# Kernel optimization log

Hardware: AMD Instinct MI355X
Metric: run time of the kernel (lower is better)

Reference implementation:

```python
import jax, jax.numpy as jnp
import numpy as np

D_MODEL = 1024
N_HEADS = 16
HEAD_DIM = D_MODEL // N_HEADS  # 64
TOP_K = 64
EPS = 1e-12  # matches F.normalize eps


def setup_inputs() -> dict:
    key = jax.random.key(0)
    ks = jax.random.split(key, 6)
    s = 0.02
    def w(k):
        return jax.random.normal(k, (D_MODEL, D_MODEL), jnp.float32) * s
    zb = jnp.zeros((D_MODEL,), jnp.float32)
    # x: (B, T, d_model); T must equal d_model (see compress_proj constraint)
    x = jax.random.normal(ks[0], (2, 1024, D_MODEL), jnp.float32)
    return {
        "x": x,
        "Wq": w(ks[1]), "bq": zb,
        "Wk": w(ks[2]), "bk": zb,
        "Wv": w(ks[3]), "bv": zb,
        "Wo": w(ks[4]), "bo": zb,
        "Wc": w(ks[5]), "bc": zb,  # compress_proj (applied along time axis)
    }


def _l2norm(a):
    n = jnp.linalg.norm(a, axis=-1, keepdims=True)
    return a / jnp.maximum(n, EPS)


def reference(x, Wq, bq, Wk, bk, Wv, bv, Wo, bo, Wc, bc):
    B, T, Dm = x.shape
    H, hd = N_HEADS, HEAD_DIM

    def proj(W, b):
        return (x @ W.T + b).reshape(B, T, H, hd).transpose(0, 2, 1, 3)  # (B,H,T,hd)

    Q = proj(Wq, bq)
    K = proj(Wk, bk)
    V = proj(Wv, bv)

    # compress_kv with compress_ratio=1: compress_proj acts on the (transposed)
    # time axis, so K_comp[b,h,c,d] = sum_t K[b,h,t,d] * Wc[c,t] + bc[c]
    K_comp = jnp.einsum('bhtd,ct->bhcd', K, Wc) + bc[None, None, :, None]
    V_comp = jnp.einsum('bhtd,ct->bhcd', V, Wc) + bc[None, None, :, None]

    # lightning indexer: cosine similarity + top-k over compressed slots
    sim = jnp.einsum('bhtd,bhcd->bhtc', _l2norm(Q), _l2norm(K_comp))
    topk_idx = jax.lax.top_k(sim, TOP_K)[1]  # (B,H,T,K)

    bi = jnp.arange(B)[:, None, None, None]
    hi = jnp.arange(H)[None, :, None, None]
    K_sel = K_comp[bi, hi, topk_idx]  # (B,H,T,K,hd)
    V_sel = V_comp[bi, hi, topk_idx]

    scores = jnp.einsum('bhtd,bhtkd->bhtk', Q, K_sel) / float(np.sqrt(hd))
    attn = jax.nn.softmax(scores, axis=-1)
    out = jnp.einsum('bhtk,bhtkd->bhtd', attn, V_sel)  # (B,H,T,hd)
    out = out.transpose(0, 2, 1, 3).reshape(B, T, Dm)
    return out @ Wo.T + bo
```

## Files before the change

kernel.cpp:

```cpp
#include <hip/hip_runtime.h>
#include <type_traits>


#define DEVI __device__ __forceinline__

constexpr int Tn = 1024;
constexpr int Cn = 1024;
constexpr int Hn = 16;

typedef short bf16x8 __attribute__((ext_vector_type(8)));
typedef float f32x4 __attribute__((ext_vector_type(4)));

DEVI int wsumi(int v)   { for (int m = 1; m < 64; m <<= 1) v += __shfl_xor(v, m); return v; }
DEVI int wmini(int v)   { for (int m = 1; m < 64; m <<= 1) { int o = __shfl_xor(v, m); v = o < v ? o : v; } return v; }
DEVI float wfmax(float v){ for (int m = 1; m < 64; m <<= 1) v = fmaxf(v, __shfl_xor(v, m)); return v; }
DEVI float wfsum(float v){ for (int m = 1; m < 64; m <<= 1) v += __shfl_xor(v, m); return v; }

DEVI unsigned long long mapd(double x) {
  unsigned long long b = (unsigned long long)__double_as_longlong(x);
  return (b >> 63) ? ~b : (b | 0x8000000000000000ull);
}

DEVI unsigned short f2bf_rne(float x) {
  unsigned u = __float_as_uint(x);
  u += 0x7fffu + ((u >> 16) & 1u);
  return (unsigned short)(u >> 16);
}
struct BfPair { short hi, lo; };
DEVI BfPair split2(float x) {
  unsigned short h = f2bf_rne(x);
  float hf = __uint_as_float(((unsigned)h) << 16);
  BfPair r;
  r.hi = (short)h;
  r.lo = (short)f2bf_rne(x - hf);
  return r;
}

template <typename OUTT, typename ACCT, bool BTRANS, int BIASMODE, bool SIM>
__global__ __launch_bounds__(256) void gemm_k(
    const float* __restrict__ A, const float* __restrict__ B,
    const float* __restrict__ bias, OUTT* __restrict__ C,
    int Kd, int lda, int ldb, int ldc,
    long long zA, long long zB, long long zC, int group_base)
{
  __shared__ float As[16][68];
  __shared__ float Bs[16][68];

  size_t offA, offB, offC;
  if (SIM) {
    int pair = group_base + (int)blockIdx.z;
    int bb = pair >> 4, hh = pair & 15;
    offA = ((size_t)bb * Tn) * (size_t)lda + (size_t)hh * 64;
    offB = ((size_t)bb * Cn) * (size_t)ldb + (size_t)hh * 64;
    offC = (size_t)blockIdx.z * (size_t)Tn * (size_t)ldc;
  } else {
    offA = (size_t)blockIdx.z * (size_t)zA;
    offB = (size_t)blockIdx.z * (size_t)zB;
    offC = (size_t)blockIdx.z * (size_t)zC;
  }
  const float* Ab = A + offA;
  const float* Bb = B + offB;
  OUTT* Cb = C + offC;

  const int tid = threadIdx.x;
  const int tx = tid & 15, ty = tid >> 4;
  const int m0 = blockIdx.y * 64, n0 = blockIdx.x * 64;

  ACCT acc[4][4];
#pragma unroll
  for (int i = 0; i < 4; ++i)
#pragma unroll
    for (int j = 0; j < 4; ++j) acc[i][j] = (ACCT)0;

  for (int k0 = 0; k0 < Kd; k0 += 16) {
    {
      int m = tid >> 2, kf = tid & 3;
      float4 a = *(const float4*)(Ab + (size_t)(m0 + m) * lda + k0 + 4 * kf);
      As[4 * kf + 0][m] = a.x; As[4 * kf + 1][m] = a.y;
      As[4 * kf + 2][m] = a.z; As[4 * kf + 3][m] = a.w;
    }
    if (BTRANS) {
      int n = tid >> 2, kf = tid & 3;
      float4 b = *(const float4*)(Bb + (size_t)(n0 + n) * ldb + k0 + 4 * kf);
      Bs[4 * kf + 0][n] = b.x; Bs[4 * kf + 1][n] = b.y;
      Bs[4 * kf + 2][n] = b.z; Bs[4 * kf + 3][n] = b.w;
    } else {
      int k = tid >> 4, nf = tid & 15;
      float4 b = *(const float4*)(Bb + (size_t)(k0 + k) * ldb + n0 + 4 * nf);
      *(float4*)&Bs[k][4 * nf] = b;
    }
    __syncthreads();
#pragma unroll
    for (int k = 0; k < 16; ++k) {
      float4 a4 = *(const float4*)&As[k][4 * ty];
      float4 b4 = *(const float4*)&Bs[k][4 * tx];
      float av[4] = {a4.x, a4.y, a4.z, a4.w};
      float bv[4] = {b4.x, b4.y, b4.z, b4.w};
#pragma unroll
      for (int i = 0; i < 4; ++i)
#pragma unroll
        for (int j = 0; j < 4; ++j)
          acc[i][j] += (ACCT)av[i] * (ACCT)bv[j];
    }
    __syncthreads();
  }

  if constexpr (std::is_same<OUTT, double>::value) {
#pragma unroll
    for (int i = 0; i < 4; ++i) {
      size_t m = (size_t)(m0 + 4 * ty + i);
      double* p = (double*)Cb + m * ldc + n0 + 4 * tx;
      p[0] = (double)acc[i][0]; p[1] = (double)acc[i][1];
      p[2] = (double)acc[i][2]; p[3] = (double)acc[i][3];
    }
  } else {
    float cbv[4] = {0.f, 0.f, 0.f, 0.f};
    if (BIASMODE == 1) {
      float4 b4 = *(const float4*)(bias + n0 + 4 * tx);
      cbv[0] = b4.x; cbv[1] = b4.y; cbv[2] = b4.z; cbv[3] = b4.w;
    }
#pragma unroll
    for (int i = 0; i < 4; ++i) {
      int m = m0 + 4 * ty + i;
      float rb = (BIASMODE == 2) ? bias[m] : 0.f;
      float4 s;
      s.x = (float)acc[i][0] + cbv[0] + rb;
      s.y = (float)acc[i][1] + cbv[1] + rb;
      s.z = (float)acc[i][2] + cbv[2] + rb;
      s.w = (float)acc[i][3] + cbv[3] + rb;
      *(float4*)((float*)Cb + (size_t)m * ldc + n0 + 4 * tx) = s;
    }
  }
}

__global__ __launch_bounds__(256) void presplit2_k(
    const float* __restrict__ src, short* __restrict__ hi,
    short* __restrict__ lo, int n8)
{
  int stride = (int)gridDim.x * 256;
  for (int i = (int)blockIdx.x * 256 + (int)threadIdx.x; i < n8; i += stride) {
    float4 v0 = ((const float4*)src)[2 * i];
    float4 v1 = ((const float4*)src)[2 * i + 1];
    BfPair q0 = split2(v0.x), q1 = split2(v0.y), q2 = split2(v0.z), q3 = split2(v0.w);
    BfPair q4 = split2(v1.x), q5 = split2(v1.y), q6 = split2(v1.z), q7 = split2(v1.w);
    bf16x8 h = {q0.hi, q1.hi, q2.hi, q3.hi, q4.hi, q5.hi, q6.hi, q7.hi};
    bf16x8 l = {q0.lo, q1.lo, q2.lo, q3.lo, q4.lo, q5.lo, q6.lo, q7.lo};
    ((bf16x8*)hi)[i] = h;
    ((bf16x8*)lo)[i] = l;
  }
}

__global__ __launch_bounds__(256) void bfgemm_k(
    const short* __restrict__ Ahi, const short* __restrict__ Alo,
    const short* __restrict__ Bhi, const short* __restrict__ Blo,
    const float* __restrict__ bias, float* __restrict__ C,
    int Kd, int lda, int ldb, int ldc)
{
  __shared__ short Ah[4 * 64 * 8];
  __shared__ short Al[4 * 64 * 8];
  __shared__ short Bh[4 * 64 * 8];
  __shared__ short Bl[4 * 64 * 8];

  const int tid = threadIdx.x;
  const int lane = tid & 63, w = tid >> 6;
  const int wr = w >> 1, wc = w & 1;
  const int m0 = blockIdx.y * 64, n0 = blockIdx.x * 64;
  const int r16 = lane & 15, kg = lane >> 4;

  f32x4 acc[2][2];
#pragma unroll
  for (int i = 0; i < 2; ++i)
#pragma unroll
    for (int j = 0; j < 2; ++j) acc[i][j] = (f32x4){0.f, 0.f, 0.f, 0.f};

  const int row = tid >> 2, kseg = tid & 3;
  const int sidx = (kseg * 64 + row) * 8;

  for (int k0 = 0; k0 < Kd; k0 += 32) {
    size_t ao = (size_t)(m0 + row) * lda + k0 + kseg * 8;
    size_t bo = (size_t)(n0 + row) * ldb + k0 + kseg * 8;
    *(bf16x8*)&Ah[sidx] = *(const bf16x8*)(Ahi + ao);
    *(bf16x8*)&Al[sidx] = *(const bf16x8*)(Alo + ao);
    *(bf16x8*)&Bh[sidx] = *(const bf16x8*)(Bhi + bo);
    *(bf16x8*)&Bl[sidx] = *(const bf16x8*)(Blo + bo);
    __syncthreads();

    bf16x8 ah[2], al[2], bh[2], bl[2];
#pragma unroll
    for (int f = 0; f < 2; ++f) {
      int ia = (kg * 64 + wr * 32 + f * 16 + r16) * 8;
      int ib = (kg * 64 + wc * 32 + f * 16 + r16) * 8;
      ah[f] = *(const bf16x8*)&Ah[ia];
      al[f] = *(const bf16x8*)&Al[ia];
      bh[f] = *(const bf16x8*)&Bh[ib];
      bl[f] = *(const bf16x8*)&Bl[ib];
    }
#pragma unroll
    for (int fr = 0; fr < 2; ++fr)
#pragma unroll
      for (int fc = 0; fc < 2; ++fc) {
        f32x4 c = acc[fr][fc];
        c = __builtin_amdgcn_mfma_f32_16x16x32_bf16(al[fr], bh[fc], c, 0, 0, 0);
        c = __builtin_amdgcn_mfma_f32_16x16x32_bf16(ah[fr], bl[fc], c, 0, 0, 0);
        c = __builtin_amdgcn_mfma_f32_16x16x32_bf16(ah[fr], bh[fc], c, 0, 0, 0);
        acc[fr][fc] = c;
      }
    __syncthreads();
  }

#pragma unroll
  for (int fr = 0; fr < 2; ++fr)
#pragma unroll
    for (int fc = 0; fc < 2; ++fc) {
      int col = n0 + wc * 32 + fc * 16 + r16;
      float cb = bias[col];
#pragma unroll
      for (int rr = 0; rr < 4; ++rr) {
        int rw = m0 + wr * 32 + fr * 16 + kg * 4 + rr;
        C[(size_t)rw * ldc + col] = acc[fr][fc][rr] + cb;
      }
    }
}

template <bool BTRANS, int BIASMODE>
__global__ __launch_bounds__(256) void mfma_gemm_k(
    const float* __restrict__ A, const float* __restrict__ B,
    const float* __restrict__ bias, float* __restrict__ C,
    int Kd, int lda, int ldb, int ldc, long long zB, long long zC)
{
  __shared__ short Ah[4 * 64 * 8];
  __shared__ short Al[4 * 64 * 8];
  __shared__ short Bh[4 * 64 * 8];
  __shared__ short Bl[4 * 64 * 8];

  const float* Bz = B + (size_t)blockIdx.z * (size_t)zB;
  float* Cz = C + (size_t)blockIdx.z * (size_t)zC;

  const int tid = threadIdx.x;
  const int lane = tid & 63, w = tid >> 6;
  const int wr = w >> 1, wc = w & 1;
  const int m0 = blockIdx.y * 64, n0 = blockIdx.x * 64;
  const int r16 = lane & 15, kg = lane >> 4;

  f32x4 acc[2][2];
#pragma unroll
  for (int i = 0; i < 2; ++i)
#pragma unroll
    for (int j = 0; j < 2; ++j) acc[i][j] = (f32x4){0.f, 0.f, 0.f, 0.f};

  for (int k0 = 0; k0 < Kd; k0 += 32) {
    {
      int row = tid >> 2, kseg = tid & 3;
      const float* p = A + (size_t)(m0 + row) * lda + k0 + kseg * 8;
      float4 v0 = *(const float4*)p;
      float4 v1 = *(const float4*)(p + 4);
      BfPair q0 = split2(v0.x), q1 = split2(v0.y), q2 = split2(v0.z), q3 = split2(v0.w);
      BfPair q4 = split2(v1.x), q5 = split2(v1.y), q6 = split2(v1.z), q7 = split2(v1.w);
      bf16x8 h = {q0.hi, q1.hi, q2.hi, q3.hi, q4.hi, q5.hi, q6.hi, q7.hi};
      bf16x8 l = {q0.lo, q1.lo, q2.lo, q3.lo, q4.lo, q5.lo, q6.lo, q7.lo};
      int idx = (kseg * 64 + row) * 8;
      *(bf16x8*)&Ah[idx] = h;
      *(bf16x8*)&Al[idx] = l;
    }
    if (BTRANS) {
      int row = tid >> 2, kseg = tid & 3;
      const float* p = Bz + (size_t)(n0 + row) * ldb + k0 + kseg * 8;
      float4 v0 = *(const float4*)p;
      float4 v1 = *(const float4*)(p + 4);
      BfPair q0 = split2(v0.x), q1 = split2(v0.y), q2 = split2(v0.z), q3 = split2(v0.w);
      BfPair q4 = split2(v1.x), q5 = split2(v1.y), q6 = split2(v1.z), q7 = split2(v1.w);
      bf16x8 h = {q0.hi, q1.hi, q2.hi, q3.hi, q4.hi, q5.hi, q6.hi, q7.hi};
      bf16x8 l = {q0.lo, q1.lo, q2.lo, q3.lo, q4.lo, q5.lo, q6.lo, q7.lo};
      int idx = (kseg * 64 + row) * 8;
      *(bf16x8*)&Bh[idx] = h;
      *(bf16x8*)&Bl[idx] = l;
    } else {
      int col = tid & 63, kseg = tid >> 6;
      short hv[8], lv[8];
#pragma unroll
      for (int j = 0; j < 8; ++j) {
        BfPair p = split2(Bz[(size_t)(k0 + kseg * 8 + j) * ldb + n0 + col]);
        hv[j] = p.hi; lv[j] = p.lo;
      }
      bf16x8 h = {hv[0], hv[1], hv[2], hv[3], hv[4], hv[5], hv[6], hv[7]};
      bf16x8 l = {lv[0], lv[1], lv[2], lv[3], lv[4], lv[5], lv[6], lv[7]};
      int idx = (kseg * 64 + col) * 8;
      *(bf16x8*)&Bh[idx] = h;
      *(bf16x8*)&Bl[idx] = l;
    }
    __syncthreads();

    bf16x8 ah[2], al[2], bh[2], bl[2];
#pragma unroll
    for (int f = 0; f < 2; ++f) {
      int ia = (kg * 64 + wr * 32 + f * 16 + r16) * 8;
      int ib = (kg * 64 + wc * 32 + f * 16 + r16) * 8;
      ah[f] = *(const bf16x8*)&Ah[ia];
      al[f] = *(const bf16x8*)&Al[ia];
      bh[f] = *(const bf16x8*)&Bh[ib];
      bl[f] = *(const bf16x8*)&Bl[ib];
    }
#pragma unroll
    for (int fr = 0; fr < 2; ++fr)
#pragma unroll
      for (int fc = 0; fc < 2; ++fc) {
        f32x4 c = acc[fr][fc];
        c = __builtin_amdgcn_mfma_f32_16x16x32_bf16(al[fr], bh[fc], c, 0, 0, 0);
        c = __builtin_amdgcn_mfma_f32_16x16x32_bf16(ah[fr], bl[fc], c, 0, 0, 0);
        c = __builtin_amdgcn_mfma_f32_16x16x32_bf16(ah[fr], bh[fc], c, 0, 0, 0);
        acc[fr][fc] = c;
      }
    __syncthreads();
  }

#pragma unroll
  for (int fr = 0; fr < 2; ++fr)
#pragma unroll
    for (int fc = 0; fc < 2; ++fc) {
      int col = n0 + wc * 32 + fc * 16 + r16;
      float cb = (BIASMODE == 1) ? bias[col] : 0.f;
#pragma unroll
      for (int rr = 0; rr < 4; ++rr) {
        int rw = m0 + wr * 32 + fr * 16 + kg * 4 + rr;
        float rb = (BIASMODE == 2) ? bias[rw] : 0.f;
        Cz[(size_t)rw * ldc + col] = acc[fr][fc][rr] + cb + rb;
      }
    }
}

__global__ __launch_bounds__(256) void kn_k2(const float* __restrict__ Kc,
                                             double* __restrict__ kn)
{
  int idx = (int)blockIdx.x * 256 + (int)threadIdx.x;
  int c = idx & 1023;
  int p = idx >> 10;
  int b = p >> 4, h = p & 15;
  const float* row = Kc + ((size_t)(b * 1024 + c)) * 1024 + h * 64;
  double s = 0.0;
  for (int d = 0; d < 64; ++d) { double v = (double)row[d]; s += v * v; }
  kn[(size_t)p * 1024 + c] = 1.0 / fmax(sqrt(s), 1e-12);
}

template <bool SPLITOUT>
__global__ __launch_bounds__(256) void topk_attn_k(
    const double* __restrict__ dotb, const double* __restrict__ kn,
    const float* __restrict__ Vc, float* __restrict__ atF,
    short* __restrict__ atHi, short* __restrict__ atLo, int group_base)
{
  __shared__ int sC[4][64];
  __shared__ float sD[4][64];

  const int lane = threadIdx.x & 63, wv = threadIdx.x >> 6;
  const int g = (int)blockIdx.x >> 8;
  const int t = ((int)blockIdx.x & 255) * 4 + wv;
  const int pair = group_base + g;
  const int bb = pair >> 4, hh = pair & 15;

  const double* drow = dotb + ((size_t)g * Tn + t) * (size_t)Cn;
  const double* knr  = kn + ((size_t)(bb * Hn + hh)) * Cn;

  double dv[16];
  unsigned long long u[16];
#pragma unroll
  for (int j = 0; j < 8; ++j) {
    double2 dd = *(const double2*)(drow + j * 128 + 2 * lane);
    double2 kk = *(const double2*)(knr  + j * 128 + 2 * lane);
    dv[2 * j] = dd.x; dv[2 * j + 1] = dd.y;
    u[2 * j]     = mapd(dd.x * kk.x);
    u[2 * j + 1] = mapd(dd.y * kk.y);
  }
  unsigned hi[16];
#pragma unroll
  for (int i = 0; i < 16; ++i) hi[i] = (unsigned)(u[i] >> 32);

  unsigned TH = 0;
  for (int bit = 31; bit >= 0; --bit) {
    unsigned Tc = TH | (1u << bit);
    int c = 0;
#pragma unroll
    for (int i = 0; i < 16; ++i) c += (hi[i] >= Tc);
    if (wsumi(c) >= 64) TH = Tc;
  }
  int mhi = 0;
#pragma unroll
  for (int i = 0; i < 16; ++i) mhi += (hi[i] > TH);
  mhi = wsumi(mhi);
  const int need1 = 64 - mhi;
  unsigned TL = 0;
  for (int bit = 31; bit >= 0; --bit) {
    unsigned Tc = TL | (1u << bit);
    int c = 0;
#pragma unroll
    for (int i = 0; i < 16; ++i) c += (hi[i] == TH && (unsigned)u[i] >= Tc);
    if (wsumi(c) >= need1) TL = Tc;
  }
  const unsigned long long V64 = ((unsigned long long)TH << 32) | TL;

  int base = 0;
#pragma unroll
  for (int i = 0; i < 16; ++i) {
    const int cix = 128 * (i >> 1) + 2 * lane + (i & 1);
    bool sel = (u[i] > V64);
    unsigned long long mk = __ballot(sel);
    if (sel) {
      int r = __popcll(mk & ((1ull << lane) - 1ull));
      sC[wv][base + r] = cix;
      sD[wv][base + r] = (float)dv[i];
    }
    base += __popcll(mk);
  }
  const int need = 64 - base;
  unsigned taken = 0;
  for (int r = 0; r < need; ++r) {
    int mn = 0x7fffffff;
#pragma unroll
    for (int i = 0; i < 16; ++i) {
      int cix = 128 * (i >> 1) + 2 * lane + (i & 1);
      if (u[i] == V64 && !((taken >> i) & 1u)) mn = mn < cix ? mn : cix;
    }
    mn = wmini(mn);
#pragma unroll
    for (int i = 0; i < 16; ++i) {
      int cix = 128 * (i >> 1) + 2 * lane + (i & 1);
      if (u[i] == V64 && !((taken >> i) & 1u) && cix == mn) {
        taken |= 1u << i;
        sC[wv][base + r] = mn;
        sD[wv][base + r] = (float)dv[i];
      }
    }
  }
  __syncthreads();

  int ck = sC[wv][lane];
  float sc = sD[wv][lane] * 0.125f;
  float mx = wfmax(sc);
  float w = expf(sc - mx);
  float sw = wfsum(w);
  w /= sw;

  const float* Vb = Vc + (size_t)bb * ((size_t)Cn * 1024) + hh * 64 + lane;
  float acc = 0.f;
#pragma unroll 4
  for (int k = 0; k < 64; ++k) {
    int c = __shfl(ck, k);
    float wk = __shfl(w, k);
    acc = fmaf(wk, Vb[(size_t)c * 1024], acc);
  }
  size_t o = ((size_t)(bb * Tn + t)) * 1024 + hh * 64 + lane;
  if (SPLITOUT) {
    BfPair p = split2(acc);
    atHi[o] = p.hi;
    atLo[o] = p.lo;
  } else {
    atF[o] = acc;
  }
}

extern "C" void kernel_launch(void* const* d_in, const int* in_sizes, int n_in,
                              void* d_out, int out_size, void* d_ws, size_t ws_size,
                              hipStream_t stream)
{
  const float* x  = (const float*)d_in[0];
  const float* Wq = (const float*)d_in[1];
  const float* bq = (const float*)d_in[2];
  const float* Wk = (const float*)d_in[3];
  const float* bk = (const float*)d_in[4];
  const float* Wv = (const float*)d_in[5];
  const float* bv = (const float*)d_in[6];
  const float* Wo = (const float*)d_in[7];
  const float* bo = (const float*)d_in[8];
  const float* Wc = (const float*)d_in[9];
  const float* bc = (const float*)d_in[10];
  float* out = (float*)d_out;

  const size_t NE = (size_t)2048 * 1024;
  const size_t M1 = (size_t)1024 * 1024;
  float* Q   = (float*)d_ws;
  float* Kf  = Q + NE;
  float* Vf  = Kf + NE;
  float* Kc  = Vf + NE;
  float* Vc  = Kc + NE;
  float* at  = Vc + NE;
  double* kn = (double*)(at + NE);
  short* Wsp = (short*)(kn + 32768);
  double* tail = (double*)(Wsp + 2 * M1);

  short* xhi = (short*)at;
  short* xlo = xhi + NE;
  short* athi = (short*)at;
  short* atlo = athi + NE;
  short* Whi = Wsp;
  short* Wlo = Wsp + M1;

  const size_t fixedB = 6 * NE * 4 + 32768 * 8;
  const size_t dotPairB = (size_t)Tn * Cn * 8;
  if (ws_size < fixedB) return;
  const bool TA = ws_size >= fixedB + ((size_t)1 << 22);

  dim3 blk(256, 1, 1);

  gemm_k<float, double, true, 1, false><<<dim3(16, 32, 1), blk, 0, stream>>>(
      x, Wq, bq, Q, 1024, 1024, 1024, 1024, 0, 0, 0, 0);
  gemm_k<float, double, true, 1, false><<<dim3(16, 32, 1), blk, 0, stream>>>(
      x, Wk, bk, Kf, 1024, 1024, 1024, 1024, 0, 0, 0, 0);

  if (TA) {
    presplit2_k<<<dim3(1024), blk, 0, stream>>>(x, xhi, xlo, (int)(NE / 8));
    presplit2_k<<<dim3(512), blk, 0, stream>>>(Wv, Whi, Wlo, (int)(M1 / 8));
    bfgemm_k<<<dim3(16, 32, 1), blk, 0, stream>>>(
        xhi, xlo, Whi, Wlo, bv, Vf, 1024, 1024, 1024, 1024);
  } else {
    mfma_gemm_k<true, 1><<<dim3(16, 32, 1), blk, 0, stream>>>(
        x, Wv, bv, Vf, 1024, 1024, 1024, 1024, 0, 0);
  }

  gemm_k<float, double, false, 2, false><<<dim3(16, 16, 2), blk, 0, stream>>>(
      Wc, Kf, bc, Kc, 1024, 1024, 1024, 1024, 0, (long long)M1, (long long)M1, 0);
  mfma_gemm_k<false, 2><<<dim3(16, 16, 2), blk, 0, stream>>>(
      Wc, Vf, bc, Vc, 1024, 1024, 1024, 1024, (long long)M1, (long long)M1);

  kn_k2<<<dim3(128), blk, 0, stream>>>(Kc, kn);

  size_t tailOff = TA ? (fixedB + ((size_t)1 << 22)) : fixedB;
  size_t rem = ws_size - tailOff;
  double* dotp; int G;
  double* tl = TA ? tail : (double*)((char*)d_ws + fixedB);
  if      (rem >= 8 * dotPairB) { G = 8; dotp = tl; }
  else if (rem >= 4 * dotPairB) { G = 4; dotp = tl; }
  else if (rem >= 2 * dotPairB) { G = 2; dotp = tl; }
  else { G = 2; dotp = (double*)Kf; }

  for (int gb = 0; gb < 32; gb += G) {
    gemm_k<double, double, true, 0, true><<<dim3(16, 16, G), blk, 0, stream>>>(
        Q, Kc, nullptr, dotp, 64, 1024, 1024, 1024, 0, 0, 0, gb);
    if (TA)
      topk_attn_k<true><<<dim3(256 * G), blk, 0, stream>>>(
          dotp, kn, Vc, nullptr, athi, atlo, gb);
    else
      topk_attn_k<false><<<dim3(256 * G), blk, 0, stream>>>(
          dotp, kn, Vc, at, nullptr, nullptr, gb);
  }

  if (TA) {
    presplit2_k<<<dim3(512), blk, 0, stream>>>(Wo, Whi, Wlo, (int)(M1 / 8));
    bfgemm_k<<<dim3(16, 32, 1), blk, 0, stream>>>(
        athi, atlo, Whi, Wlo, bo, out, 1024, 1024, 1024, 1024);
  } else {
    mfma_gemm_k<true, 1><<<dim3(16, 32, 1), blk, 0, stream>>>(
        at, Wo, bo, out, 1024, 1024, 1024, 1024, 0, 0);
  }
}
```

Baseline: 960.8 us.

## Use FP64 MFMA for double-precision GEMMs with runtime layout detection

```diff
diff --git a/kernel.cpp b/kernel.cpp
--- a/kernel.cpp
+++ b/kernel.cpp
@@ -10,6 +10,7 @@
 
 typedef short bf16x8 __attribute__((ext_vector_type(8)));
 typedef float f32x4 __attribute__((ext_vector_type(4)));
+typedef double f64x4 __attribute__((ext_vector_type(4)));
 
 DEVI int wsumi(int v)   { for (int m = 1; m < 64; m <<= 1) v += __shfl_xor(v, m); return v; }
 DEVI int wmini(int v)   { for (int m = 1; m < 64; m <<= 1) { int o = __shfl_xor(v, m); v = o < v ? o : v; } return v; }
@@ -36,17 +37,17 @@
   return r;
 }
 
-template <typename OUTT, typename ACCT, bool BTRANS, int BIASMODE, bool SIM>
-__global__ __launch_bounds__(256) void gemm_k(
+template <typename OUTT, bool BTRANS, int BIASMODE, bool SIM>
+__global__ __launch_bounds__(256) void f64sel_k(
     const float* __restrict__ A, const float* __restrict__ B,
     const float* __restrict__ bias, OUTT* __restrict__ C,
     int Kd, int lda, int ldb, int ldc,
-    long long zA, long long zB, long long zC, int group_base)
+    long long zB, long long zC, int group_base)
 {
   __shared__ float As[16][68];
   __shared__ float Bs[16][68];
 
-  size_t offA, offB, offC;
+  size_t offA = 0, offB = 0, offC = 0;
   if (SIM) {
     int pair = group_base + (int)blockIdx.z;
     int bb = pair >> 4, hh = pair & 15;
@@ -54,7 +55,6 @@
     offB = ((size_t)bb * Cn) * (size_t)ldb + (size_t)hh * 64;
     offC = (size_t)blockIdx.z * (size_t)Tn * (size_t)ldc;
   } else {
-    offA = (size_t)blockIdx.z * (size_t)zA;
     offB = (size_t)blockIdx.z * (size_t)zB;
     offC = (size_t)blockIdx.z * (size_t)zC;
   }
@@ -63,14 +63,38 @@
   OUTT* Cb = C + offC;
 
   const int tid = threadIdx.x;
-  const int tx = tid & 15, ty = tid >> 4;
+  const int lane = tid & 63, w = tid >> 6;
+  const int wr = w >> 1, wc = w & 1;
+  const int l15 = lane & 15, l4 = lane >> 4;
   const int m0 = blockIdx.y * 64, n0 = blockIdx.x * 64;
 
-  ACCT acc[4][4];
-#pragma unroll
-  for (int i = 0; i < 4; ++i)
-#pragma unroll
-    for (int j = 0; j < 4; ++j) acc[i][j] = (ACCT)0;
+  f64x4 zz = {0.0, 0.0, 0.0, 0.0};
+  f64x4 p1 = __builtin_amdgcn_mfma_f64_16x16x4f64(1.0, (double)l15, zz, 0, 0, 0);
+  f64x4 p2 = __builtin_amdgcn_mfma_f64_16x16x4f64((double)l15, 1.0, zz, 0, 0, 0);
+  int a1 = 1, b1 = 1, c1 = 1, a2 = 1, b2 = 1, c2 = 1;
+#pragma unroll
+  for (int rr = 0; rr < 4; ++rr) {
+    a1 &= (p1[rr] == 4.0 * l15);
+    b1 &= (p1[rr] == 4.0 * (l4 * 4 + rr));
+    c1 &= (p1[rr] == 4.0 * (l4 + 4 * rr));
+    a2 &= (p2[rr] == 4.0 * (l4 * 4 + rr));
+    b2 &= (p2[rr] == 4.0 * (l4 + 4 * rr));
+    c2 &= (p2[rr] == 4.0 * l15);
+  }
+  a1 = __all(a1); b1 = __all(b1); c1 = __all(c1);
+  a2 = __all(a2); b2 = __all(b2); c2 = __all(c2);
+  int dmap = 0, useM = 1;
+  if      (a1 && a2) dmap = 0;
+  else if (a1 && b2) dmap = 1;
+  else if (b1 && c2) dmap = 2;
+  else if (c1 && c2) dmap = 3;
+  else useM = 0;
+
+  f64x4 acc[2][2];
+#pragma unroll
+  for (int i = 0; i < 2; ++i)
+#pragma unroll
+    for (int j = 0; j < 2; ++j) acc[i][j] = (f64x4){0.0, 0.0, 0.0, 0.0};
 
   for (int k0 = 0; k0 < Kd; k0 += 16) {
     {
@@ -90,47 +114,61 @@
       *(float4*)&Bs[k][4 * nf] = b;
     }
     __syncthreads();
-#pragma unroll
-    for (int k = 0; k < 16; ++k) {
-      float4 a4 = *(const float4*)&As[k][4 * ty];
-      float4 b4 = *(const float4*)&Bs[k][4 * tx];
-      float av[4] = {a4.x, a4.y, a4.z, a4.w};
-      float bv[4] = {b4.x, b4.y, b4.z, b4.w};
-#pragma unroll
-      for (int i = 0; i < 4; ++i)
-#pragma unroll
-        for (int j = 0; j < 4; ++j)
-          acc[i][j] += (ACCT)av[i] * (ACCT)bv[j];
+
+    if (useM) {
+#pragma unroll
+      for (int kq = 0; kq < 4; ++kq) {
+        int kk = kq * 4 + l4;
+        double a0  = (double)As[kk][wr * 32 + l15];
+        double a1v = (double)As[kk][wr * 32 + 16 + l15];
+        double b0  = (double)Bs[kk][wc * 32 + l15];
+        double b1v = (double)Bs[kk][wc * 32 + 16 + l15];
+        acc[0][0] = __builtin_amdgcn_mfma_f64_16x16x4f64(a0,  b0,  acc[0][0], 0, 0, 0);
+        acc[0][1] = __builtin_amdgcn_mfma_f64_16x16x4f64(a0,  b1v, acc[0][1], 0, 0, 0);
+        acc[1][0] = __builtin_amdgcn_mfma_f64_16x16x4f64(a1v, b0,  acc[1][0], 0, 0, 0);
+        acc[1][1] = __builtin_amdgcn_mfma_f64_16x16x4f64(a1v, b1v, acc[1][1], 0, 0, 0);
+      }
+    } else {
+#pragma unroll
+      for (int k = 0; k < 16; ++k) {
+        double bv0 = (double)Bs[k][wc * 32 + l15];
+        double bv1 = (double)Bs[k][wc * 32 + 16 + l15];
+#pragma unroll
+        for (int fr = 0; fr < 2; ++fr)
+#pragma unroll
+          for (int rr = 0; rr < 4; ++rr) {
+            double av = (double)As[k][wr * 32 + fr * 16 + l4 * 4 + rr];
+            acc[fr][0][rr] += av * bv0;
+            acc[fr][1][rr] += av * bv1;
+          }
+      }
     }
     __syncthreads();
   }
 
-  if constexpr (std::is_same<OUTT, double>::value) {
-#pragma unroll
-    for (int i = 0; i < 4; ++i) {
-      size_t m = (size_t)(m0 + 4 * ty + i);
-      double* p = (double*)Cb + m * ldc + n0 + 4 * tx;
-      p[0] = (double)acc[i][0]; p[1] = (double)acc[i][1];
-      p[2] = (double)acc[i][2]; p[3] = (double)acc[i][3];
-    }
-  } else {
-    float cbv[4] = {0.f, 0.f, 0.f, 0.f};
-    if (BIASMODE == 1) {
-      float4 b4 = *(const float4*)(bias + n0 + 4 * tx);
-      cbv[0] = b4.x; cbv[1] = b4.y; cbv[2] = b4.z; cbv[3] = b4.w;
-    }
-#pragma unroll
-    for (int i = 0; i < 4; ++i) {
-      int m = m0 + 4 * ty + i;
-      float rb = (BIASMODE == 2) ? bias[m] : 0.f;
-      float4 s;
-      s.x = (float)acc[i][0] + cbv[0] + rb;
-      s.y = (float)acc[i][1] + cbv[1] + rb;
-      s.z = (float)acc[i][2] + cbv[2] + rb;
-      s.w = (float)acc[i][3] + cbv[3] + rb;
-      *(float4*)((float*)Cb + (size_t)m * ldc + n0 + 4 * tx) = s;
-    }
-  }
+#pragma unroll
+  for (int fr = 0; fr < 2; ++fr)
+#pragma unroll
+    for (int fc = 0; fc < 2; ++fc)
+#pragma unroll
+      for (int rr = 0; rr < 4; ++rr) {
+        int ri, ci;
+        if (!useM || dmap == 0) { ri = l4 * 4 + rr; ci = l15; }
+        else if (dmap == 1)     { ri = l4 + 4 * rr; ci = l15; }
+        else if (dmap == 2)     { ri = l15; ci = l4 * 4 + rr; }
+        else                    { ri = l15; ci = l4 + 4 * rr; }
+        int row = m0 + wr * 32 + fr * 16 + ri;
+        int col = n0 + wc * 32 + fc * 16 + ci;
+        double v = acc[fr][fc][rr];
+        if constexpr (std::is_same<OUTT, double>::value) {
+          Cb[(size_t)row * ldc + col] = v;
+        } else {
+          float s = (float)v;
+          float cb = (BIASMODE == 1) ? bias[col] : 0.f;
+          float rb = (BIASMODE == 2) ? bias[row] : 0.f;
+          ((float*)Cb)[(size_t)row * ldc + col] = s + cb + rb;
+        }
+      }
 }
 
 __global__ __launch_bounds__(256) void presplit2_k(
@@ -499,10 +537,10 @@
 
   dim3 blk(256, 1, 1);
 
-  gemm_k<float, double, true, 1, false><<<dim3(16, 32, 1), blk, 0, stream>>>(
-      x, Wq, bq, Q, 1024, 1024, 1024, 1024, 0, 0, 0, 0);
-  gemm_k<float, double, true, 1, false><<<dim3(16, 32, 1), blk, 0, stream>>>(
-      x, Wk, bk, Kf, 1024, 1024, 1024, 1024, 0, 0, 0, 0);
+  f64sel_k<float, true, 1, false><<<dim3(16, 32, 1), blk, 0, stream>>>(
+      x, Wq, bq, Q, 1024, 1024, 1024, 1024, 0, 0, 0);
+  f64sel_k<float, true, 1, false><<<dim3(16, 32, 1), blk, 0, stream>>>(
+      x, Wk, bk, Kf, 1024, 1024, 1024, 1024, 0, 0, 0);
 
   if (TA) {
     presplit2_k<<<dim3(1024), blk, 0, stream>>>(x, xhi, xlo, (int)(NE / 8));
@@ -514,8 +552,8 @@
         x, Wv, bv, Vf, 1024, 1024, 1024, 1024, 0, 0);
   }
 
-  gemm_k<float, double, false, 2, false><<<dim3(16, 16, 2), blk, 0, stream>>>(
-      Wc, Kf, bc, Kc, 1024, 1024, 1024, 1024, 0, (long long)M1, (long long)M1, 0);
+  f64sel_k<float, false, 2, false><<<dim3(16, 16, 2), blk, 0, stream>>>(
+      Wc, Kf, bc, Kc, 1024, 1024, 1024, 1024, (long long)M1, (long long)M1, 0);
   mfma_gemm_k<false, 2><<<dim3(16, 16, 2), blk, 0, stream>>>(
       Wc, Vf, bc, Vc, 1024, 1024, 1024, 1024, (long long)M1, (long long)M1);
 
@@ -531,8 +569,8 @@
   else { G = 2; dotp = (double*)Kf; }
 
   for (int gb = 0; gb < 32; gb += G) {
-    gemm_k<double, double, true, 0, true><<<dim3(16, 16, G), blk, 0, stream>>>(
-        Q, Kc, nullptr, dotp, 64, 1024, 1024, 1024, 0, 0, 0, gb);
+    f64sel_k<double, true, 0, true><<<dim3(16, 16, G), blk, 0, stream>>>(
+        Q, Kc, nullptr, dotp, 64, 1024, 1024, 1024, 0, 0, gb);
     if (TA)
       topk_attn_k<true><<<dim3(256 * G), blk, 0, stream>>>(
           dotp, kn, Vc, nullptr, athi, atlo, gb);
```

After: 882.2 us. -8.2%, faster.
